# Kernel optimization log

Measured on AMD Instinct MI355X. Metric: run time of the kernel, lower is better.

Reference implementation:

```python
import jax, jax.numpy as jnp
import numpy as np

B, GRID, SPACING, RADIUS = 32, 8, 2.0, 3.5
CODE, H, L = 1024, 128, 4
N_GRID = GRID ** 3  # 512 nodes per sample
N = B * N_GRID      # 16384 total nodes


def _build_graph():
    # deterministic anchor grid (centered) + radius graph, replicated per batch sample
    ax = (np.arange(GRID) - (GRID - 1) / 2.0) * SPACING
    g = np.stack(np.meshgrid(ax, ax, ax, indexing='ij'), -1).reshape(-1, 3).astype(np.float32)
    d2 = ((g[:, None, :] - g[None, :, :]) ** 2).sum(-1)
    row, col = np.nonzero((d2 <= RADIUS ** 2) & (d2 > 1e-8))  # no self loops
    off = (np.arange(B) * N_GRID)[:, None]
    rows = (row[None, :] + off).reshape(-1)
    cols = (col[None, :] + off).reshape(-1)
    coords = np.tile(g, (B, 1))
    return jnp.asarray(coords), jnp.asarray(np.stack([rows, cols]).astype(np.int32))


def setup_inputs() -> dict:
    key = jax.random.key(0)
    ks = jax.random.split(key, 8)
    coords, edge_index = _build_graph()
    def lin(k, fi, fo):
        return jax.random.normal(k, (fi, fo), jnp.float32) / np.float32(np.sqrt(fi))
    return {
        'y': jax.random.normal(ks[0], (B, N_GRID, CODE), jnp.float32),
        'grid_coords': coords,
        'edge_index': edge_index,
        'W_in': lin(ks[1], CODE, H), 'b_in': jnp.zeros((H,), jnp.float32),
        'ln_g': jnp.ones((L, H), jnp.float32), 'ln_b': jnp.zeros((L, H), jnp.float32),
        'eW1': jax.random.normal(ks[2], (L, 2 * H + 1, H), jnp.float32) / np.float32(np.sqrt(2 * H + 1)),
        'eb1': jnp.zeros((L, H), jnp.float32),
        'eW2': jax.random.normal(ks[3], (L, H, H), jnp.float32) / np.float32(np.sqrt(H)),
        'eb2': jnp.zeros((L, H), jnp.float32),
        'nW1': jax.random.normal(ks[4], (L, 2 * H, H), jnp.float32) / np.float32(np.sqrt(2 * H)),
        'nb1': jnp.zeros((L, H), jnp.float32),
        'nW2': jax.random.normal(ks[5], (L, H, H), jnp.float32) / np.float32(np.sqrt(H)),
        'nb2': jnp.zeros((L, H), jnp.float32),
        'W_out': lin(ks[6], H, CODE), 'b_out': jnp.zeros((CODE,), jnp.float32),
    }


def _layer_norm(x, g, b, eps=1e-5):
    mu = jnp.mean(x, -1, keepdims=True)
    v = jnp.mean((x - mu) ** 2, -1, keepdims=True)
    return (x - mu) * jax.lax.rsqrt(v + eps) * g + b


def reference(y, grid_coords, edge_index, W_in, b_in, ln_g, ln_b,
              eW1, eb1, eW2, eb2, nW1, nb1, nW2, nb2, W_out, b_out):
    row, col = edge_index[0], edge_index[1]
    rel = grid_coords[col] - grid_coords[row]               # [E,3]
    dist = jnp.sqrt(jnp.sum(rel * rel, -1, keepdims=True))  # [E,1]
    n_nodes = grid_coords.shape[0]
    deg = jnp.maximum(
        jax.ops.segment_sum(jnp.ones(col.shape, jnp.float32), col, num_segments=n_nodes), 1.0)
    h = (y @ W_in + b_in).reshape(n_nodes, H)               # input projection
    for l in range(L):
        hn = _layer_norm(h, ln_g[l], ln_b[l])
        e_in = jnp.concatenate([hn[row], hn[col], dist], -1)        # [E, 2H+1]
        m = jax.nn.silu(e_in @ eW1[l] + eb1[l])
        m = jax.nn.silu(m @ eW2[l] + eb2[l])                        # [E, H]
        agg = jax.ops.segment_sum(m, col, num_segments=n_nodes) / deg[:, None]  # scatter-mean
        hd = jax.nn.silu(jnp.concatenate([hn, agg], -1) @ nW1[l] + nb1[l])
        hd = hd @ nW2[l] + nb2[l]
        h = hn + hd                                                  # residual from normed h
    return h.reshape(B, N_GRID, H) @ W_out + b_out                   # [B, 512, 1024]
```

## Files before the change

kernel.cpp:

```cpp
#include <hip/hip_runtime.h>
#include <math.h>

#define NN 16384
#define H 128
#define CODE 1024
#define RSTR 132

typedef __attribute__((ext_vector_type(8))) short short8;
typedef __attribute__((ext_vector_type(4))) float f32x4;

#define OFF_WIN   0u
#define OFF_WOUT  262144u
#define OFF_P     524288u
#define OFF_N1    786432u
#define OFF_N2    1048576u
#define OFF_W2    1179648u
#define OFF_H     1318912u
#define OFF_HN    (OFF_H + 8388608u)
#define OFF_PBUF  (OFF_HN + 8388608u)

__device__ __forceinline__ float silu(float x) { return x / (1.0f + __expf(-x)); }

__device__ __forceinline__ unsigned short f2bf(float f) {
    unsigned int u = __float_as_uint(f);
    u = (u + 0x7FFFu + ((u >> 16) & 1u)) >> 16;
    return (unsigned short)u;
}

__device__ __forceinline__ float bf2f(short s) {
    return __uint_as_float(((unsigned)(unsigned short)s) << 16);
}

__device__ __forceinline__ short8 pack_bf16_8(const float* v) {
    union { unsigned u[4]; short8 s; } r;
    asm("v_cvt_pk_bf16_f32 %0, %1, %2" : "=v"(r.u[0]) : "v"(v[0]), "v"(v[1]));
    asm("v_cvt_pk_bf16_f32 %0, %1, %2" : "=v"(r.u[1]) : "v"(v[2]), "v"(v[3]));
    asm("v_cvt_pk_bf16_f32 %0, %1, %2" : "=v"(r.u[2]) : "v"(v[4]), "v"(v[5]));
    asm("v_cvt_pk_bf16_f32 %0, %1, %2" : "=v"(r.u[3]) : "v"(v[6]), "v"(v[7]));
    return r.s;
}

__device__ __forceinline__ short8 cvtfrag(const float* p) {
    float v[8];
    float4 a = *(const float4*)p;
    float4 b = *(const float4*)(p + 4);
    v[0]=a.x; v[1]=a.y; v[2]=a.z; v[3]=a.w; v[4]=b.x; v[5]=b.y; v[6]=b.z; v[7]=b.w;
    return pack_bf16_8(v);
}

__device__ const int SDX[26] = {-1,-1,-1,-1, 1, 1, 1, 1,  -1,-1,-1,-1, 0,  0, 0, 0, 1, 1, 1, 1,  -1, 1, 0, 0, 0, 0};
__device__ const int SDY[26] = {-1,-1, 1, 1,-1,-1, 1, 1,  -1, 0, 0, 1,-1, -1, 1, 1,-1, 0, 0, 1,   0, 0,-1, 1, 0, 0};
__device__ const int SDZ[26] = {-1, 1,-1, 1,-1, 1,-1, 1,   0,-1, 1, 0,-1,  1,-1, 1, 0,-1, 1, 0,   0, 0, 0, 0,-1, 1};

__global__ void k_prep(const float* __restrict__ W_in, const float* __restrict__ W_out,
                       const float* __restrict__ eW1, const float* __restrict__ nW1,
                       const float* __restrict__ nW2, const float* __restrict__ eW2,
                       char* __restrict__ base) {
    int t = blockIdx.x * 256 + threadIdx.x;
    if (t < 131072) {
        int n = t >> 10, k = t & 1023;
        *(unsigned short*)(base + OFF_WIN + n * 2048 + k * 2) = f2bf(W_in[k * 128 + n]);
        return;
    }
    t -= 131072;
    if (t < 131072) {
        int n = t >> 7, k = t & 127;
        *(unsigned short*)(base + OFF_WOUT + n * 256 + k * 2) = f2bf(W_out[k * 1024 + n]);
        return;
    }
    t -= 131072;
    if (t < 131072) {
        int l = t >> 15, r = t & 32767;
        int jj = r >> 7, k = r & 127;
        const float* W = eW1 + (size_t)l * 257 * 128;
        float v = (jj < 128) ? W[k * 128 + jj] : W[(128 + k) * 128 + (jj - 128)];
        *(unsigned short*)(base + OFF_P + (size_t)l * 65536 + jj * 256 + k * 2) = f2bf(v);
        return;
    }
    t -= 131072;
    if (t < 131072) {
        int l = t >> 15, r = t & 32767;
        int n = r >> 8, k = r & 255;
        *(unsigned short*)(base + OFF_N1 + (size_t)l * 65536 + n * 512 + k * 2) =
            f2bf(nW1[(size_t)l * 256 * 128 + k * 128 + n]);
        return;
    }
    t -= 131072;
    if (t < 65536) {
        int l = t >> 14, r = t & 16383;
        int n = r >> 7, k = r & 127;
        *(unsigned short*)(base + OFF_N2 + (size_t)l * 32768 + n * 256 + k * 2) =
            f2bf(nW2[(size_t)l * 128 * 128 + k * 128 + n]);
        return;
    }
    t -= 65536;
    if (t < 65536) {
        int l = t >> 14, r = t & 16383;
        int n = r >> 7, k = r & 127;
        *(unsigned short*)(base + OFF_W2 + (size_t)l * 32768 + n * 256 + k * 2) =
            f2bf(eW2[(size_t)l * 128 * 128 + k * 128 + n]);
    }
}

__global__ __launch_bounds__(256) void k_in_mfma(const float* __restrict__ y,
                                                 const char* __restrict__ imgWin,
                                                 const float* __restrict__ bi,
                                                 float* __restrict__ h) {
    int tid = threadIdx.x, w = tid >> 6, lane = tid & 63;
    int l15 = lane & 15, kg = lane >> 4;
    int m0 = blockIdx.x * 64 + w * 16;
    const float* yr = y + (size_t)(m0 + l15) * CODE;
    f32x4 acc[8];
#pragma unroll
    for (int nt = 0; nt < 8; nt++) { f32x4 z = {0.f,0.f,0.f,0.f}; acc[nt] = z; }
#pragma unroll 4
    for (int ks = 0; ks < 32; ks++) {
        short8 a = cvtfrag(yr + ks * 32 + kg * 8);
        const char* bp = imgWin + ks * 64 + kg * 16;
#pragma unroll
        for (int nt = 0; nt < 8; nt++) {
            short8 b = *(const short8*)(bp + (nt * 16 + l15) * 2048);
            acc[nt] = __builtin_amdgcn_mfma_f32_16x16x32_bf16(a, b, acc[nt], 0, 0, 0);
        }
    }
#pragma unroll
    for (int nt = 0; nt < 8; nt++) {
        int cc = nt * 16 + l15;
        float bb = bi[cc];
#pragma unroll
        for (int r = 0; r < 4; r++)
            h[(size_t)(m0 + kg * 4 + r) * H + cc] = acc[nt][r] + bb;
    }
}

__global__ __launch_bounds__(256) void k_lnP(const float* __restrict__ h,
                                             const float* __restrict__ g,
                                             const float* __restrict__ bln,
                                             const char* __restrict__ imgP,
                                             const float* __restrict__ b1,
                                             float* __restrict__ hn,
                                             unsigned short* __restrict__ Pb) {
    int bid = blockIdx.x;
    int rowblk = bid >> 1, nc = bid & 1;
    int tid = threadIdx.x, w = tid >> 6, lane = tid & 63;
    int l15 = lane & 15, kg = lane >> 4;
    int m0 = rowblk * 64 + w * 16;
    int row = m0 + l15;
    const float* hr = h + (size_t)row * H;

    float hv[32];
#pragma unroll
    for (int ks = 0; ks < 4; ks++) {
        float4 a4 = *(const float4*)(hr + ks * 32 + kg * 8);
        float4 b4 = *(const float4*)(hr + ks * 32 + kg * 8 + 4);
        hv[ks*8+0]=a4.x; hv[ks*8+1]=a4.y; hv[ks*8+2]=a4.z; hv[ks*8+3]=a4.w;
        hv[ks*8+4]=b4.x; hv[ks*8+5]=b4.y; hv[ks*8+6]=b4.z; hv[ks*8+7]=b4.w;
    }
    float s = 0.0f;
#pragma unroll
    for (int i = 0; i < 32; i++) s += hv[i];
    s += __shfl_xor(s, 16); s += __shfl_xor(s, 32);
    float mu = s * (1.0f / 128.0f);
    float vs = 0.0f;
#pragma unroll
    for (int i = 0; i < 32; i++) { float d = hv[i] - mu; vs += d * d; }
    vs += __shfl_xor(vs, 16); vs += __shfl_xor(vs, 32);
    float rs = rsqrtf(vs * (1.0f / 128.0f) + 1e-5f);

#pragma unroll
    for (int ks = 0; ks < 4; ks++) {
        float4 g0 = *(const float4*)(g + ks * 32 + kg * 8);
        float4 g1 = *(const float4*)(g + ks * 32 + kg * 8 + 4);
        float4 c0 = *(const float4*)(bln + ks * 32 + kg * 8);
        float4 c1 = *(const float4*)(bln + ks * 32 + kg * 8 + 4);
        hv[ks*8+0] = (hv[ks*8+0]-mu)*rs*g0.x + c0.x;
        hv[ks*8+1] = (hv[ks*8+1]-mu)*rs*g0.y + c0.y;
        hv[ks*8+2] = (hv[ks*8+2]-mu)*rs*g0.z + c0.z;
        hv[ks*8+3] = (hv[ks*8+3]-mu)*rs*g0.w + c0.w;
        hv[ks*8+4] = (hv[ks*8+4]-mu)*rs*g1.x + c1.x;
        hv[ks*8+5] = (hv[ks*8+5]-mu)*rs*g1.y + c1.y;
        hv[ks*8+6] = (hv[ks*8+6]-mu)*rs*g1.z + c1.z;
        hv[ks*8+7] = (hv[ks*8+7]-mu)*rs*g1.w + c1.w;
    }
    if (nc == 0) {
        float* o = hn + (size_t)row * H;
#pragma unroll
        for (int ks = 0; ks < 4; ks++) {
            *(float4*)(o + ks * 32 + kg * 8)     = *(float4*)&hv[ks*8];
            *(float4*)(o + ks * 32 + kg * 8 + 4) = *(float4*)&hv[ks*8+4];
        }
    }
    short8 a[4];
#pragma unroll
    for (int ks = 0; ks < 4; ks++) a[ks] = pack_bf16_8(&hv[ks*8]);

    f32x4 acc[8];
#pragma unroll
    for (int nt = 0; nt < 8; nt++) { f32x4 z = {0.f,0.f,0.f,0.f}; acc[nt] = z; }
#pragma unroll
    for (int ks = 0; ks < 4; ks++) {
        const char* bp = imgP + (size_t)(nc * 128) * 256 + ks * 64 + kg * 16;
#pragma unroll
        for (int nt = 0; nt < 8; nt++) {
            short8 b = *(const short8*)(bp + (nt * 16 + l15) * 256);
            acc[nt] = __builtin_amdgcn_mfma_f32_16x16x32_bf16(a[ks], b, acc[nt], 0, 0, 0);
        }
    }
#pragma unroll
    for (int nt = 0; nt < 8; nt++) {
        int jj = nc * 128 + nt * 16 + l15;
        float add = nc ? b1[nt * 16 + l15] : 0.0f;
#pragma unroll
        for (int r = 0; r < 4; r++)
            Pb[(size_t)(m0 + kg * 4 + r) * 256 + jj] = f2bf(acc[nt][r] + add);
    }
}

__global__ __launch_bounds__(512) void k_layer(
        const unsigned short* __restrict__ Pb, const char* __restrict__ imgW2,
        const float* __restrict__ w256f, const float* __restrict__ b2,
        float* __restrict__ hn, const char* __restrict__ imgN1,
        const float* __restrict__ nb1, const char* __restrict__ imgN2,
        const float* __restrict__ nb2, float* __restrict__ h, int last,
        const float* __restrict__ lngn, const float* __restrict__ lnbn,
        const char* __restrict__ imgPn, const float* __restrict__ b1n,
        unsigned short* __restrict__ PbOut) {
    __shared__ __align__(16) char sP1[3 * 12288];
    __shared__ __align__(16) char sB[32768];
    float* red = (float*)sB;

    int tid = threadIdx.x, wv = tid >> 6, lane = tid & 63;
    int mt = wv & 1, grp = wv >> 1;
    int l15 = lane & 15, kg = lane >> 4;
    int n0 = blockIdx.x * 32;
    int x = (n0 >> 6) & 7;
    int y0 = (n0 >> 3) & 7;

#pragma unroll
    for (int i = 0; i < 5; i++) {
        int u = tid + i * 512;
        if (u < 2304) {
            int p = u / 768, rem = u - p * 768;
            int lr = rem >> 4, unit = rem & 15;
            int j = lr >> 3, zz = lr & 7;
            int xp = x + p - 1, yp = y0 - 1 + j;
            if (((unsigned)xp < 8u) & ((unsigned)yp < 8u)) {
                const char* src = (const char*)Pb +
                    (size_t)(n0 + (p - 1) * 64 + (j - 1) * 8 + zz) * 512 + unit * 16;
                *(uint4*)(sP1 + p * 12288 + lr * 256 + ((unit ^ (lr & 15)) << 4)) =
                    *(const uint4*)src;
            }
        }
    }
#pragma unroll
    for (int i = 0; i < 4; i++) {
        int u = tid + i * 512;
        int row = u >> 4, unit = u & 15;
        *(uint4*)(sB + row * 256 + ((unit ^ (row & 15)) << 4)) =
            *(const uint4*)(imgW2 + row * 256 + unit * 16);
    }
    __syncthreads();

    int rowbase = mt * 16 + l15;
    int yrel = rowbase >> 3, za = rowbase & 7;
    int ya = y0 + yrel;

    float p2f[32], wf[32];
    const char* p2p = (const char*)Pb + (size_t)(n0 + rowbase) * 512 + 256;
#pragma unroll
    for (int ks = 0; ks < 4; ks++) {
        short8 s = *(const short8*)(p2p + ks * 64 + kg * 16);
#pragma unroll
        for (int i = 0; i < 8; i++) p2f[ks * 8 + i] = bf2f(s[i]);
        float4 a4 = *(const float4*)(w256f + ks * 32 + kg * 8);
        float4 b4 = *(const float4*)(w256f + ks * 32 + kg * 8 + 4);
        wf[ks*8+0]=a4.x; wf[ks*8+1]=a4.y; wf[ks*8+2]=a4.z; wf[ks*8+3]=a4.w;
        wf[ks*8+4]=b4.x; wf[ks*8+5]=b4.y; wf[ks*8+6]=b4.z; wf[ks*8+7]=b4.w;
    }
    float b2v[8];
#pragma unroll
    for (int nt = 0; nt < 8; nt++) b2v[nt] = b2[nt * 16 + l15];

    float accag[8][4];
#pragma unroll
    for (int nt = 0; nt < 8; nt++)
#pragma unroll
        for (int r = 0; r < 4; r++) accag[nt][r] = 0.0f;

    int ye = y0 + mt * 2 + (kg >> 1), ze = (kg & 1) * 4;

    for (int o = grp; o < 26; o += 4) {
        int dx = SDX[o], dy = SDY[o], dz = SDZ[o];
        if ((unsigned)(x + dx) >= 8u) continue;
        float d = sqrtf((float)(4 * (dx * dx + dy * dy + dz * dz)));
        bool va = ((unsigned)(ya + dy) < 8u) & ((unsigned)(za + dz) < 8u);
        int lr = va ? ((yrel + dy + 1) * 8 + za + dz) : ((yrel + 1) * 8 + za);
        const char* ap = sP1 + (dx + 1) * 12288 + lr * 256;
        int rsw = lr & 15;

        f32x4 c[8];
#pragma unroll
        for (int nt = 0; nt < 8; nt++) { f32x4 z4 = {0.f,0.f,0.f,0.f}; c[nt] = z4; }
#pragma unroll
        for (int ks = 0; ks < 4; ks++) {
            short8 s = *(const short8*)(ap + (((ks * 4 + kg) ^ rsw) << 4));
            float vv[8];
#pragma unroll
            for (int i = 0; i < 8; i++) {
                float v = bf2f(s[i]) + p2f[ks * 8 + i] + d * wf[ks * 8 + i];
                vv[i] = silu(v);
            }
            short8 a = pack_bf16_8(vv);
            __builtin_amdgcn_s_setprio(1);
#pragma unroll
            for (int nt = 0; nt < 8; nt++) {
                int brow = nt * 16 + l15;
                short8 b = *(const short8*)(sB + brow * 256 + (((ks * 4 + kg) ^ l15) << 4));
                c[nt] = __builtin_amdgcn_mfma_f32_16x16x32_bf16(a, b, c[nt], 0, 0, 0);
            }
            __builtin_amdgcn_s_setprio(0);
        }
#pragma unroll
        for (int r = 0; r < 4; r++) {
            bool vr = ((unsigned)(ye + dy) < 8u) & ((unsigned)(ze + r + dz) < 8u);
#pragma unroll
            for (int nt = 0; nt < 8; nt++) {
                float v = silu(c[nt][r] + b2v[nt]);
                accag[nt][r] += vr ? v : 0.0f;
            }
        }
    }

    __syncthreads();
    if (grp == 0) {
#pragma unroll
        for (int nt = 0; nt < 8; nt++)
#pragma unroll
            for (int r = 0; r < 4; r++)
                red[(mt * 16 + kg * 4 + r) * RSTR + nt * 16 + l15] = accag[nt][r];
    }
    __syncthreads();
    if (grp == 1) {
#pragma unroll
        for (int nt = 0; nt < 8; nt++)
#pragma unroll
            for (int r = 0; r < 4; r++)
                red[(mt * 16 + kg * 4 + r) * RSTR + nt * 16 + l15] += accag[nt][r];
    }
    __syncthreads();
    if (grp == 2) {
#pragma unroll
        for (int nt = 0; nt < 8; nt++)
#pragma unroll
            for (int r = 0; r < 4; r++)
                red[(mt * 16 + kg * 4 + r) * RSTR + nt * 16 + l15] += accag[nt][r];
    }
    __syncthreads();
    if (grp == 3) {
#pragma unroll
        for (int nt = 0; nt < 8; nt++)
#pragma unroll
            for (int r = 0; r < 4; r++)
                red[(mt * 16 + kg * 4 + r) * RSTR + nt * 16 + l15] += accag[nt][r];
    }
    __syncthreads();

    int nodeA = n0 + rowbase;
    int yA = (nodeA >> 3) & 7, zA = nodeA & 7;
    float dinvA = 1.0f / (float)((1 + (x > 0) + (x < 7)) * (1 + (yA > 0) + (yA < 7))
                                 * (1 + (zA > 0) + (zA < 7)) - 1);
    const float* hnr = hn + (size_t)nodeA * H;
    f32x4 acc1[2];
    { f32x4 z = {0.f,0.f,0.f,0.f}; acc1[0] = z; acc1[1] = z; }
#pragma unroll
    for (int ks = 0; ks < 8; ks++) {
        short8 a;
        if (ks < 4) a = cvtfrag(hnr + ks * 32 + kg * 8);
        else {
            float vv[8];
            const float* rp = red + rowbase * RSTR + (ks - 4) * 32 + kg * 8;
#pragma unroll
            for (int i = 0; i < 8; i++) vv[i] = rp[i] * dinvA;
            a = pack_bf16_8(vv);
        }
        const char* bp = imgN1 + ks * 64 + kg * 16;
#pragma unroll
        for (int t = 0; t < 2; t++) {
            short8 b = *(const short8*)(bp + ((grp * 2 + t) * 16 + l15) * 512);
            acc1[t] = __builtin_amdgcn_mfma_f32_16x16x32_bf16(a, b, acc1[t], 0, 0, 0);
        }
    }
    char* sM = sP1;
#pragma unroll
    for (int t = 0; t < 2; t++) {
        int cc = (grp * 2 + t) * 16 + l15;
        float bb = nb1[cc];
#pragma unroll
        for (int r = 0; r < 4; r++) {
            float v = silu(acc1[t][r] + bb);
            *(unsigned short*)(sM + (mt * 16 + kg * 4 + r) * 272 + cc * 2) = f2bf(v);
        }
    }
    __syncthreads();

    f32x4 acc2[2];
    { f32x4 z = {0.f,0.f,0.f,0.f}; acc2[0] = z; acc2[1] = z; }
#pragma unroll
    for (int ks = 0; ks < 4; ks++) {
        short8 a = *(const short8*)(sM + rowbase * 272 + ks * 64 + kg * 16);
        const char* bp = imgN2 + ks * 64 + kg * 16;
#pragma unroll
        for (int t = 0; t < 2; t++) {
            short8 b = *(const short8*)(bp + ((grp * 2 + t) * 16 + l15) * 256);
            acc2[t] = __builtin_amdgcn_mfma_f32_16x16x32_bf16(a, b, acc2[t], 0, 0, 0);
        }
    }
    float* h2 = (float*)sB;
#pragma unroll
    for (int t = 0; t < 2; t++) {
        int cc = (grp * 2 + t) * 16 + l15;
        float bb = nb2[cc];
#pragma unroll
        for (int r = 0; r < 4; r++) {
            int rr = mt * 16 + kg * 4 + r;
            size_t gi = (size_t)(n0 + rr) * H + cc;
            float v = hn[gi] + acc2[t][r] + bb;
            if (last) h[gi] = v;
            else      h2[rr * RSTR + cc] = v;
        }
    }
    if (last) return;
    __syncthreads();

    float hv[32];
    const float* h2r = h2 + rowbase * RSTR;
#pragma unroll
    for (int ks = 0; ks < 4; ks++) {
#pragma unroll
        for (int i = 0; i < 8; i++) hv[ks * 8 + i] = h2r[ks * 32 + kg * 8 + i];
    }
    float s = 0.0f;
#pragma unroll
    for (int i = 0; i < 32; i++) s += hv[i];
    s += __shfl_xor(s, 16); s += __shfl_xor(s, 32);
    float mu = s * (1.0f / 128.0f);
    float vs = 0.0f;
#pragma unroll
    for (int i = 0; i < 32; i++) { float d = hv[i] - mu; vs += d * d; }
    vs += __shfl_xor(vs, 16); vs += __shfl_xor(vs, 32);
    float rsq = rsqrtf(vs * (1.0f / 128.0f) + 1e-5f);
#pragma unroll
    for (int ks = 0; ks < 4; ks++) {
        float4 g0 = *(const float4*)(lngn + ks * 32 + kg * 8);
        float4 g1 = *(const float4*)(lngn + ks * 32 + kg * 8 + 4);
        float4 c0 = *(const float4*)(lnbn + ks * 32 + kg * 8);
        float4 c1 = *(const float4*)(lnbn + ks * 32 + kg * 8 + 4);
        hv[ks*8+0] = (hv[ks*8+0]-mu)*rsq*g0.x + c0.x;
        hv[ks*8+1] = (hv[ks*8+1]-mu)*rsq*g0.y + c0.y;
        hv[ks*8+2] = (hv[ks*8+2]-mu)*rsq*g0.z + c0.z;
        hv[ks*8+3] = (hv[ks*8+3]-mu)*rsq*g0.w + c0.w;
        hv[ks*8+4] = (hv[ks*8+4]-mu)*rsq*g1.x + c1.x;
        hv[ks*8+5] = (hv[ks*8+5]-mu)*rsq*g1.y + c1.y;
        hv[ks*8+6] = (hv[ks*8+6]-mu)*rsq*g1.z + c1.z;
        hv[ks*8+7] = (hv[ks*8+7]-mu)*rsq*g1.w + c1.w;
    }
    if (grp == 0) {
        float* o = hn + (size_t)nodeA * H;
#pragma unroll
        for (int ks = 0; ks < 4; ks++) {
            *(float4*)(o + ks * 32 + kg * 8)     = *(float4*)&hv[ks*8];
            *(float4*)(o + ks * 32 + kg * 8 + 4) = *(float4*)&hv[ks*8+4];
        }
    }
    short8 aF[4];
#pragma unroll
    for (int ks = 0; ks < 4; ks++) aF[ks] = pack_bf16_8(&hv[ks*8]);
    f32x4 accP[4];
#pragma unroll
    for (int t = 0; t < 4; t++) { f32x4 z = {0.f,0.f,0.f,0.f}; accP[t] = z; }
#pragma unroll
    for (int ks = 0; ks < 4; ks++) {
        const char* bp = imgPn + ks * 64 + kg * 16;
#pragma unroll
        for (int t = 0; t < 4; t++) {
            int jt = grp * 4 + t;
            short8 b = *(const short8*)(bp + (jt * 16 + l15) * 256);
            accP[t] = __builtin_amdgcn_mfma_f32_16x16x32_bf16(aF[ks], b, accP[t], 0, 0, 0);
        }
    }
#pragma unroll
    for (int t = 0; t < 4; t++) {
        int jj = (grp * 4 + t) * 16 + l15;
        float add = (jj >= 128) ? b1n[jj - 128] : 0.0f;
#pragma unroll
        for (int r = 0; r < 4; r++)
            PbOut[(size_t)(n0 + mt * 16 + kg * 4 + r) * 256 + jj] = f2bf(accP[t][r] + add);
    }
}

__global__ __launch_bounds__(256) void k_out_mfma(const float* __restrict__ h,
                                                  const char* __restrict__ imgWout,
                                                  const float* __restrict__ bo,
                                                  float* __restrict__ out) {
    int bid = blockIdx.x;
    int rowblk = bid >> 3, nc = bid & 7;
    int tid = threadIdx.x, w = tid >> 6, lane = tid & 63;
    int l15 = lane & 15, kg = lane >> 4;
    int m0 = rowblk * 64 + w * 16;
    const float* hr = h + (size_t)(m0 + l15) * H;
    short8 a[4];
#pragma unroll
    for (int ks = 0; ks < 4; ks++) a[ks] = cvtfrag(hr + ks * 32 + kg * 8);
    f32x4 acc[8];
#pragma unroll
    for (int nt = 0; nt < 8; nt++) { f32x4 z = {0.f,0.f,0.f,0.f}; acc[nt] = z; }
#pragma unroll
    for (int ks = 0; ks < 4; ks++) {
        const char* bp = imgWout + (size_t)(nc * 128) * 256 + ks * 64 + kg * 16;
#pragma unroll
        for (int nt = 0; nt < 8; nt++) {
            short8 b = *(const short8*)(bp + (nt * 16 + l15) * 256);
            acc[nt] = __builtin_amdgcn_mfma_f32_16x16x32_bf16(a[ks], b, acc[nt], 0, 0, 0);
        }
    }
#pragma unroll
    for (int nt = 0; nt < 8; nt++) {
        int cc = nc * 128 + nt * 16 + l15;
        float bb = bo[cc];
#pragma unroll
        for (int r = 0; r < 4; r++)
            out[(size_t)(m0 + kg * 4 + r) * 1024 + cc] = acc[nt][r] + bb;
    }
}

extern "C" void kernel_launch(void* const* d_in, const int* in_sizes, int n_in,
                              void* d_out, int out_size, void* d_ws, size_t ws_size,
                              hipStream_t stream) {
    const float* y     = (const float*)d_in[0];
    const float* W_in  = (const float*)d_in[3];
    const float* b_in  = (const float*)d_in[4];
    const float* ln_g  = (const float*)d_in[5];
    const float* ln_b  = (const float*)d_in[6];
    const float* eW1   = (const float*)d_in[7];
    const float* eb1   = (const float*)d_in[8];
    const float* eW2   = (const float*)d_in[9];
    const float* eb2   = (const float*)d_in[10];
    const float* nW1   = (const float*)d_in[11];
    const float* nb1   = (const float*)d_in[12];
    const float* nW2   = (const float*)d_in[13];
    const float* nb2   = (const float*)d_in[14];
    const float* W_out = (const float*)d_in[15];
    const float* b_out = (const float*)d_in[16];

    char* wsb = (char*)d_ws;
    float* h    = (float*)(wsb + OFF_H);
    float* hn   = (float*)(wsb + OFF_HN);
    unsigned short* PbA = (unsigned short*)(wsb + OFF_PBUF);
    unsigned short* PbB = PbA + 4194304;

    k_prep<<<655360 / 256, 256, 0, stream>>>(W_in, W_out, eW1, nW1, nW2, eW2, wsb);
    k_in_mfma<<<NN / 64, 256, 0, stream>>>(y, wsb + OFF_WIN, b_in, h);
    k_lnP<<<NN / 64 * 2, 256, 0, stream>>>(h, ln_g, ln_b, wsb + OFF_P, eb1, hn, PbA);
    for (int l = 0; l < 4; ++l) {
        const unsigned short* Pin = (l & 1) ? PbB : PbA;
        unsigned short* Pout      = (l & 1) ? PbA : PbB;
        int last = (l == 3);
        int ln = last ? 0 : (l + 1);
        k_layer<<<NN / 32, 512, 0, stream>>>(
            Pin, wsb + OFF_W2 + (size_t)l * 32768,
            eW1 + (size_t)l * 257 * H + 256 * H, eb2 + l * H,
            hn, wsb + OFF_N1 + (size_t)l * 65536, nb1 + l * H,
            wsb + OFF_N2 + (size_t)l * 32768, nb2 + l * H,
            h, last,
            ln_g + ln * H, ln_b + ln * H,
            wsb + OFF_P + (size_t)ln * 65536, eb1 + ln * H, Pout);
    }
    k_out_mfma<<<NN / 64 * 8, 256, 0, stream>>>(h, wsb + OFF_WOUT, b_out, (float*)d_out);
}
```

Baseline: 544.5 us.

## Process a whole x-slab of 64 nodes per block with 12 waves

```diff
diff --git a/kernel.cpp b/kernel.cpp
--- a/kernel.cpp
+++ b/kernel.cpp
@@ -216,7 +216,7 @@
     }
 }
 
-__global__ __launch_bounds__(512) void k_layer(
+__global__ __launch_bounds__(768) void k_layer(
         const unsigned short* __restrict__ Pb, const char* __restrict__ imgW2,
         const float* __restrict__ w256f, const float* __restrict__ b2,
         float* __restrict__ hn, const char* __restrict__ imgN1,
@@ -225,45 +225,42 @@
         const float* __restrict__ lngn, const float* __restrict__ lnbn,
         const char* __restrict__ imgPn, const float* __restrict__ b1n,
         unsigned short* __restrict__ PbOut) {
-    __shared__ __align__(16) char sP1[3 * 12288];
+    __shared__ __align__(16) char sP1[3 * 16384];
     __shared__ __align__(16) char sB[32768];
-    float* red = (float*)sB;
+    float* red = (float*)sP1;
+    float* h2  = (float*)sP1;
+    char*  sM  = sB;
 
     int tid = threadIdx.x, wv = tid >> 6, lane = tid & 63;
-    int mt = wv & 1, grp = wv >> 1;
+    int mt = wv & 3, grp = wv >> 2;
     int l15 = lane & 15, kg = lane >> 4;
-    int n0 = blockIdx.x * 32;
+    int n0 = blockIdx.x * 64;
     int x = (n0 >> 6) & 7;
-    int y0 = (n0 >> 3) & 7;
-
-#pragma unroll
-    for (int i = 0; i < 5; i++) {
-        int u = tid + i * 512;
-        if (u < 2304) {
-            int p = u / 768, rem = u - p * 768;
-            int lr = rem >> 4, unit = rem & 15;
-            int j = lr >> 3, zz = lr & 7;
-            int xp = x + p - 1, yp = y0 - 1 + j;
-            if (((unsigned)xp < 8u) & ((unsigned)yp < 8u)) {
-                const char* src = (const char*)Pb +
-                    (size_t)(n0 + (p - 1) * 64 + (j - 1) * 8 + zz) * 512 + unit * 16;
-                *(uint4*)(sP1 + p * 12288 + lr * 256 + ((unit ^ (lr & 15)) << 4)) =
-                    *(const uint4*)src;
-            }
-        }
-    }
+
 #pragma unroll
     for (int i = 0; i < 4; i++) {
-        int u = tid + i * 512;
-        int row = u >> 4, unit = u & 15;
-        *(uint4*)(sB + row * 256 + ((unit ^ (row & 15)) << 4)) =
-            *(const uint4*)(imgW2 + row * 256 + unit * 16);
+        int u = tid + i * 768;
+        int p = u >> 10, rem = u & 1023;
+        int row = rem >> 4, unit = rem & 15;
+        int xp = x + p - 1;
+        if ((unsigned)xp < 8u) {
+            const char* src = (const char*)Pb + (size_t)(n0 + (p - 1) * 64 + row) * 512 + unit * 16;
+            *(uint4*)(sP1 + p * 16384 + row * 256 + ((unit ^ (row & 15)) << 4)) = *(const uint4*)src;
+        }
+    }
+#pragma unroll
+    for (int i = 0; i < 3; i++) {
+        int u = tid + i * 768;
+        if (u < 2048) {
+            int row = u >> 4, unit = u & 15;
+            *(uint4*)(sB + row * 256 + ((unit ^ (row & 15)) << 4)) =
+                *(const uint4*)(imgW2 + row * 256 + unit * 16);
+        }
     }
     __syncthreads();
 
     int rowbase = mt * 16 + l15;
-    int yrel = rowbase >> 3, za = rowbase & 7;
-    int ya = y0 + yrel;
+    int ya = rowbase >> 3, za = rowbase & 7;
 
     float p2f[32], wf[32];
     const char* p2p = (const char*)Pb + (size_t)(n0 + rowbase) * 512 + 256;
@@ -287,16 +284,16 @@
 #pragma unroll
         for (int r = 0; r < 4; r++) accag[nt][r] = 0.0f;
 
-    int ye = y0 + mt * 2 + (kg >> 1), ze = (kg & 1) * 4;
-
-    for (int o = grp; o < 26; o += 4) {
+    int ye = mt * 2 + (kg >> 1), ze = (kg & 1) * 4;
+
+    for (int o = grp; o < 26; o += 3) {
         int dx = SDX[o], dy = SDY[o], dz = SDZ[o];
         if ((unsigned)(x + dx) >= 8u) continue;
         float d = sqrtf((float)(4 * (dx * dx + dy * dy + dz * dz)));
         bool va = ((unsigned)(ya + dy) < 8u) & ((unsigned)(za + dz) < 8u);
-        int lr = va ? ((yrel + dy + 1) * 8 + za + dz) : ((yrel + 1) * 8 + za);
-        const char* ap = sP1 + (dx + 1) * 12288 + lr * 256;
-        int rsw = lr & 15;
+        int rowr = va ? (rowbase + dy * 8 + dz) : rowbase;
+        const char* ap = sP1 + (dx + 1) * 16384 + rowr * 256;
+        int rsw = rowr & 15;
 
         f32x4 c[8];
 #pragma unroll
@@ -349,14 +346,6 @@
     }
     __syncthreads();
     if (grp == 2) {
-#pragma unroll
-        for (int nt = 0; nt < 8; nt++)
-#pragma unroll
-            for (int r = 0; r < 4; r++)
-                red[(mt * 16 + kg * 4 + r) * RSTR + nt * 16 + l15] += accag[nt][r];
-    }
-    __syncthreads();
-    if (grp == 3) {
 #pragma unroll
         for (int nt = 0; nt < 8; nt++)
 #pragma unroll
@@ -370,8 +359,9 @@
     float dinvA = 1.0f / (float)((1 + (x > 0) + (x < 7)) * (1 + (yA > 0) + (yA < 7))
                                  * (1 + (zA > 0) + (zA < 7)) - 1);
     const float* hnr = hn + (size_t)nodeA * H;
-    f32x4 acc1[2];
-    { f32x4 z = {0.f,0.f,0.f,0.f}; acc1[0] = z; acc1[1] = z; }
+    f32x4 acc1[3];
+#pragma unroll
+    for (int t = 0; t < 3; t++) { f32x4 z = {0.f,0.f,0.f,0.f}; acc1[t] = z; }
 #pragma unroll
     for (int ks = 0; ks < 8; ks++) {
         short8 a;
@@ -385,48 +375,59 @@
         }
         const char* bp = imgN1 + ks * 64 + kg * 16;
 #pragma unroll
-        for (int t = 0; t < 2; t++) {
-            short8 b = *(const short8*)(bp + ((grp * 2 + t) * 16 + l15) * 512);
-            acc1[t] = __builtin_amdgcn_mfma_f32_16x16x32_bf16(a, b, acc1[t], 0, 0, 0);
-        }
-    }
-    char* sM = sP1;
-#pragma unroll
-    for (int t = 0; t < 2; t++) {
-        int cc = (grp * 2 + t) * 16 + l15;
-        float bb = nb1[cc];
-#pragma unroll
-        for (int r = 0; r < 4; r++) {
-            float v = silu(acc1[t][r] + bb);
-            *(unsigned short*)(sM + (mt * 16 + kg * 4 + r) * 272 + cc * 2) = f2bf(v);
-        }
-    }
-    __syncthreads();
-
-    f32x4 acc2[2];
-    { f32x4 z = {0.f,0.f,0.f,0.f}; acc2[0] = z; acc2[1] = z; }
+        for (int t = 0; t < 3; t++) {
+            int nt = grp + 3 * t;
+            if (nt < 8) {
+                short8 b = *(const short8*)(bp + (nt * 16 + l15) * 512);
+                acc1[t] = __builtin_amdgcn_mfma_f32_16x16x32_bf16(a, b, acc1[t], 0, 0, 0);
+            }
+        }
+    }
+#pragma unroll
+    for (int t = 0; t < 3; t++) {
+        int nt = grp + 3 * t;
+        if (nt < 8) {
+            int cc = nt * 16 + l15;
+            float bb = nb1[cc];
+#pragma unroll
+            for (int r = 0; r < 4; r++) {
+                float v = silu(acc1[t][r] + bb);
+                *(unsigned short*)(sM + (mt * 16 + kg * 4 + r) * 272 + cc * 2) = f2bf(v);
+            }
+        }
+    }
+    __syncthreads();
+
+    f32x4 acc2[3];
+#pragma unroll
+    for (int t = 0; t < 3; t++) { f32x4 z = {0.f,0.f,0.f,0.f}; acc2[t] = z; }
 #pragma unroll
     for (int ks = 0; ks < 4; ks++) {
         short8 a = *(const short8*)(sM + rowbase * 272 + ks * 64 + kg * 16);
         const char* bp = imgN2 + ks * 64 + kg * 16;
 #pragma unroll
-        for (int t = 0; t < 2; t++) {
-            short8 b = *(const short8*)(bp + ((grp * 2 + t) * 16 + l15) * 256);
-            acc2[t] = __builtin_amdgcn_mfma_f32_16x16x32_bf16(a, b, acc2[t], 0, 0, 0);
-        }
-    }
-    float* h2 = (float*)sB;
-#pragma unroll
-    for (int t = 0; t < 2; t++) {
-        int cc = (grp * 2 + t) * 16 + l15;
-        float bb = nb2[cc];
-#pragma unroll
-        for (int r = 0; r < 4; r++) {
-            int rr = mt * 16 + kg * 4 + r;
-            size_t gi = (size_t)(n0 + rr) * H + cc;
-            float v = hn[gi] + acc2[t][r] + bb;
-            if (last) h[gi] = v;
-            else      h2[rr * RSTR + cc] = v;
+        for (int t = 0; t < 3; t++) {
+            int nt = grp + 3 * t;
+            if (nt < 8) {
+                short8 b = *(const short8*)(bp + (nt * 16 + l15) * 256);
+                acc2[t] = __builtin_amdgcn_mfma_f32_16x16x32_bf16(a, b, acc2[t], 0, 0, 0);
+            }
+        }
+    }
+#pragma unroll
+    for (int t = 0; t < 3; t++) {
+        int nt = grp + 3 * t;
+        if (nt < 8) {
+            int cc = nt * 16 + l15;
+            float bb = nb2[cc];
+#pragma unroll
+            for (int r = 0; r < 4; r++) {
+                int rr = mt * 16 + kg * 4 + r;
+                size_t gi = (size_t)(n0 + rr) * H + cc;
+                float v = hn[gi] + acc2[t][r] + bb;
+                if (last) h[gi] = v;
+                else      h2[rr * RSTR + cc] = v;
+            }
         }
     }
     if (last) return;
@@ -475,26 +476,31 @@
     short8 aF[4];
 #pragma unroll
     for (int ks = 0; ks < 4; ks++) aF[ks] = pack_bf16_8(&hv[ks*8]);
-    f32x4 accP[4];
-#pragma unroll
-    for (int t = 0; t < 4; t++) { f32x4 z = {0.f,0.f,0.f,0.f}; accP[t] = z; }
+    f32x4 accP[6];
+#pragma unroll
+    for (int t = 0; t < 6; t++) { f32x4 z = {0.f,0.f,0.f,0.f}; accP[t] = z; }
 #pragma unroll
     for (int ks = 0; ks < 4; ks++) {
         const char* bp = imgPn + ks * 64 + kg * 16;
 #pragma unroll
-        for (int t = 0; t < 4; t++) {
-            int jt = grp * 4 + t;
-            short8 b = *(const short8*)(bp + (jt * 16 + l15) * 256);
-            accP[t] = __builtin_amdgcn_mfma_f32_16x16x32_bf16(aF[ks], b, accP[t], 0, 0, 0);
-        }
-    }
-#pragma unroll
-    for (int t = 0; t < 4; t++) {
-        int jj = (grp * 4 + t) * 16 + l15;
-        float add = (jj >= 128) ? b1n[jj - 128] : 0.0f;
-#pragma unroll
-        for (int r = 0; r < 4; r++)
-            PbOut[(size_t)(n0 + mt * 16 + kg * 4 + r) * 256 + jj] = f2bf(accP[t][r] + add);
+        for (int t = 0; t < 6; t++) {
+            int jt = grp + 3 * t;
+            if (jt < 16) {
+                short8 b = *(const short8*)(bp + (jt * 16 + l15) * 256);
+                accP[t] = __builtin_amdgcn_mfma_f32_16x16x32_bf16(aF[ks], b, accP[t], 0, 0, 0);
+            }
+        }
+    }
+#pragma unroll
+    for (int t = 0; t < 6; t++) {
+        int jt = grp + 3 * t;
+        if (jt < 16) {
+            int jj = jt * 16 + l15;
+            float add = (jj >= 128) ? b1n[jj - 128] : 0.0f;
+#pragma unroll
+            for (int r = 0; r < 4; r++)
+                PbOut[(size_t)(n0 + mt * 16 + kg * 4 + r) * 256 + jj] = f2bf(accP[t][r] + add);
+        }
     }
 }
 
@@ -566,7 +572,7 @@
         unsigned short* Pout      = (l & 1) ? PbA : PbB;
         int last = (l == 3);
         int ln = last ? 0 : (l + 1);
-        k_layer<<<NN / 32, 512, 0, stream>>>(
+        k_layer<<<NN / 64, 768, 0, stream>>>(
             Pin, wsb + OFF_W2 + (size_t)l * 32768,
             eW1 + (size_t)l * 257 * H + 256 * H, eb2 + l * H,
             hn, wsb + OFF_N1 + (size_t)l * 65536, nb1 + l * H,
```

Result: faster. 531.3 us (-2.4%).
